# Kernel optimization log

Hardware: AMD Instinct MI355X
Metric: run time of the kernel (lower is better)

Reference implementation:

```python
import jax, jax.numpy as jnp
import numpy as np
from jax import lax

N, C, H, W = 32, 256, 32, 32
E, K, MLP = 8, 2, 4
CAP = 1.25
HID = MLP * C
LN_EPS = 1e-6


def setup_inputs() -> dict:
    key = jax.random.key(0)
    ks = jax.random.split(key, 12)
    s = 0.02
    return {
        "input": jax.random.normal(ks[0], (N, C, H, W), jnp.float32),
        "dw_kernel": jax.random.normal(ks[1], (C, 1, 7, 7), jnp.float32) * s,
        "dw_bias": jnp.zeros((C,), jnp.float32),
        "ln_gamma": jnp.ones((C,), jnp.float32),
        "ln_beta": jnp.zeros((C,), jnp.float32),
        "router_w": jax.random.normal(ks[2], (C, E), jnp.float32) * s,
        "w1": jax.random.normal(ks[3], (E, C, HID), jnp.float32) * s,
        "b1": jnp.zeros((E, HID), jnp.float32),
        "w2": jax.random.normal(ks[4], (E, HID, C), jnp.float32) * s,
        "b2": jnp.zeros((E, C), jnp.float32),
        "layer_scale": jnp.full((C, 1, 1), 1e-6, jnp.float32),
    }


def reference(input, dw_kernel, dw_bias, ln_gamma, ln_beta, router_w,
              w1, b1, w2, b2, layer_scale):
    # depthwise 7x7 conv (groups = C), NCHW
    x = lax.conv_general_dilated(
        input, dw_kernel, window_strides=(1, 1), padding=[(3, 3), (3, 3)],
        dimension_numbers=("NCHW", "OIHW", "NCHW"), feature_group_count=C)
    x = x + dw_bias[None, :, None, None]
    x = jnp.transpose(x, (0, 2, 3, 1))  # NHWC
    # LayerNorm over channels
    mu = jnp.mean(x, axis=-1, keepdims=True)
    var = jnp.mean(jnp.square(x - mu), axis=-1, keepdims=True)
    x = (x - mu) * lax.rsqrt(var + LN_EPS) * ln_gamma + ln_beta

    T = N * H * W
    x_flat = x.reshape(T, C)

    # router (eval mode of NoisyTopKRouter: no noise)
    logits = x_flat @ router_w                      # [T, E]
    top_logits, topi = lax.top_k(logits, K)          # [T, K]
    weights = jax.nn.softmax(top_logits, axis=-1)    # [T, K]
    priority = weights[:, 0]
    order = jnp.argsort(-priority)                   # descending priority

    # build K*T candidates, stably sorted by expert id
    token_idx = jnp.tile(order, K)                           # order.repeat(K)
    expert_id = topi[order].T.reshape(-1)
    gate_w = weights[order].T.reshape(-1)
    perm = jnp.argsort(expert_id)                            # stable
    token_idx, expert_id, gate_w = token_idx[perm], expert_id[perm], gate_w[perm]

    # capacity truncation
    Be = int(K * T * CAP / E + 0.5)
    counts = jnp.bincount(expert_id, length=E)
    starts = jnp.cumsum(counts) - counts
    pos = jnp.arange(K * T) - starts[expert_id]
    keep = pos < Be
    slot = jnp.where(keep, expert_id * Be + pos, E * Be)     # dump slot for drops

    # dispatch to capacity buffers [E, Be, C]
    buf = jnp.zeros((E * Be + 1, C), x_flat.dtype).at[slot].set(x_flat[token_idx])
    buf = buf[:E * Be].reshape(E, Be, C)

    # grouped expert MLP: Linear -> GELU(exact) -> Linear
    h = jax.nn.gelu(jnp.einsum("ebc,ech->ebh", buf, w1) + b1[:, None, :],
                    approximate=False)
    y = jnp.einsum("ebh,ehc->ebc", h, w2) + b2[:, None, :]

    # combine: gather back, gate-scale (zero for dropped), scatter-add
    y_pad = jnp.concatenate([y.reshape(E * Be, C),
                             jnp.zeros((1, C), y.dtype)], axis=0)
    contrib = y_pad[slot] * (gate_w * keep.astype(gate_w.dtype))[:, None]
    out = jnp.zeros((T, C), x_flat.dtype).at[token_idx].add(contrib)

    out = out.reshape(N, H, W, C).transpose(0, 3, 1, 2)      # NCHW
    # stochastic_depth_prob = 0 -> identity
    return input + layer_scale[None] * out
```

## Files before the change

### kernel.cpp

```cpp
#include <hip/hip_runtime.h>
#include <math.h>

#define TOK 32768
#define CH  256
#define HIDN 1024
#define NE  8
#define BE  10240
#define CNT_STRIDE 64

typedef __attribute__((ext_vector_type(8))) short bf16x8;
typedef __attribute__((ext_vector_type(4))) float f32x4;
typedef __attribute__((ext_vector_type(2))) long long2v;

__device__ __forceinline__ unsigned short f2bf(float f) {
    unsigned u = __builtin_bit_cast(unsigned, f);
    unsigned r = 0x7FFFu + ((u >> 16) & 1u);
    return (unsigned short)((u + r) >> 16);
}
__device__ __forceinline__ float bf2f(unsigned short u) {
    return __builtin_bit_cast(float, (unsigned)u << 16);
}
__device__ __forceinline__ unsigned pk8_lo(float a, float b, unsigned old) {
    return (unsigned)__builtin_amdgcn_cvt_pk_fp8_f32(a, b, (int)old, false);
}
__device__ __forceinline__ unsigned pk8_hi(float a, float b, unsigned old) {
    return (unsigned)__builtin_amdgcn_cvt_pk_fp8_f32(a, b, (int)old, true);
}
__device__ __forceinline__ f32x4 mfma8(long a, long b, f32x4 c) {
    return __builtin_amdgcn_mfma_f32_16x16x32_fp8_fp8(a, b, c, 0, 0, 0);
}

typedef __attribute__((address_space(3))) void lds_t;
typedef const __attribute__((address_space(1))) void gm_t;
#define GL16(gp, lp) __builtin_amdgcn_global_load_lds((gm_t*)(gp), (lds_t*)(lp), 16, 0, 0)

__global__ __launch_bounds__(256) void k_conv(const float* __restrict__ in,
                                              const float* __restrict__ kern,
                                              const float* __restrict__ bias,
                                              unsigned char* __restrict__ xc8,
                                              int* __restrict__ cnt) {
    __shared__ float img[1024];
    __shared__ float kwl[49];
    int t = threadIdx.x;
    int bid = blockIdx.x;
    int c = bid & 255;
    if (bid == 0) { cnt[t] = 0; cnt[t + 256] = 0; }

    GL16(in + (size_t)bid * 1024 + t * 4, (char*)img + t * 16);
    if (t < 49) kwl[t] = kern[c * 49 + t];
    __syncthreads();

    int x0 = (t & 7) * 4, y = t >> 3;
    float b0 = bias[c];
    float acc[4] = {b0, b0, b0, b0};
#pragma unroll
    for (int jr = 0; jr < 7; ++jr) {
        int yy = y + jr - 3;
        if ((unsigned)yy < 32u) {
            float row[10];
#pragma unroll
            for (int k = 0; k < 10; ++k) {
                int xx = x0 - 3 + k;
                row[k] = ((unsigned)xx < 32u) ? img[yy * 32 + xx] : 0.f;
            }
#pragma unroll
            for (int kx = 0; kx < 7; ++kx) {
                float kv = kwl[jr * 7 + kx];
#pragma unroll
                for (int o = 0; o < 4; ++o) acc[o] = fmaf(row[o + kx], kv, acc[o]);
            }
        }
    }
    unsigned u = pk8_lo(acc[0], acc[1], 0u);
    u = pk8_hi(acc[2], acc[3], u);
    *(unsigned*)(xc8 + (size_t)bid * 1024 + y * 32 + x0) = u;
}

__global__ __launch_bounds__(512) void k_lnr(const unsigned char* __restrict__ xc8,
                                             const float* __restrict__ gamma,
                                             const float* __restrict__ beta,
                                             const float* __restrict__ rw,
                                             unsigned* __restrict__ xf8,
                                             int* __restrict__ e01,
                                             float2* __restrict__ gates) {
    __shared__ float acc[32][260];
    int t = threadIdx.x;
    int n = blockIdx.x >> 5, y = blockIdx.x & 31;
    int x4 = t & 7, ch = t >> 3;

#pragma unroll
    for (int i = 0; i < 4; ++i) {
        int c = i * 64 + ch;
        unsigned word = *(const unsigned*)(xc8 + ((size_t)(n * 256 + c)) * 1024 + y * 32 + x4 * 4);
        acc[x4 * 4 + 0][c] = __builtin_amdgcn_cvt_f32_fp8((int)word, 0);
        acc[x4 * 4 + 1][c] = __builtin_amdgcn_cvt_f32_fp8((int)word, 1);
        acc[x4 * 4 + 2][c] = __builtin_amdgcn_cvt_f32_fp8((int)word, 2);
        acc[x4 * 4 + 3][c] = __builtin_amdgcn_cvt_f32_fp8((int)word, 3);
    }
    __syncthreads();

    int lane = t & 63, w = t >> 6;
    float4 g4 = ((const float4*)gamma)[lane];
    float4 b4 = ((const float4*)beta)[lane];
    int c0 = lane * 4;
    float4 rwv[8];
#pragma unroll
    for (int j = 0; j < 4; ++j) {
        rwv[j * 2]     = *(const float4*)(rw + (size_t)(c0 + j) * 8);
        rwv[j * 2 + 1] = *(const float4*)(rw + (size_t)(c0 + j) * 8 + 4);
    }

#pragma unroll
    for (int k = 0; k < 4; ++k) {
        int tl = w * 4 + k;
        float4 v = *(const float4*)&acc[tl][lane * 4];
        float s = v.x + v.y + v.z + v.w;
        float q = v.x * v.x + v.y * v.y + v.z * v.z + v.w * v.w;
#pragma unroll
        for (int m = 1; m < 64; m <<= 1) { s += __shfl_xor(s, m); q += __shfl_xor(q, m); }
        float mean = s * (1.0f / 256.0f);
        float var  = q * (1.0f / 256.0f) - mean * mean;
        float rstd = rsqrtf(var + 1e-6f);

        float xn[4];
        xn[0] = (v.x - mean) * rstd * g4.x + b4.x;
        xn[1] = (v.y - mean) * rstd * g4.y + b4.y;
        xn[2] = (v.z - mean) * rstd * g4.z + b4.z;
        xn[3] = (v.w - mean) * rstd * g4.w + b4.w;

        unsigned px = pk8_lo(xn[0], xn[1], 0u);
        px = pk8_hi(xn[2], xn[3], px);
        int tok = n * 1024 + y * 32 + tl;
        xf8[tok * 64 + lane] = px;

        float p[8];
#pragma unroll
        for (int e = 0; e < 8; ++e) p[e] = 0.f;
#pragma unroll
        for (int j = 0; j < 4; ++j) {
            float xv = xn[j];
            const float* r0 = (const float*)&rwv[j * 2];
#pragma unroll
            for (int e = 0; e < 8; ++e) p[e] += xv * r0[e];
        }
#pragma unroll
        for (int m = 1; m < 64; m <<= 1) {
#pragma unroll
            for (int e = 0; e < 8; ++e) p[e] += __shfl_xor(p[e], m);
        }
        if (lane == 0) {
            int e0 = 0; float l0 = p[0];
#pragma unroll
            for (int e = 1; e < 8; ++e) if (p[e] > l0) { l0 = p[e]; e0 = e; }
            int e1 = -1; float l1 = -3.4e38f;
#pragma unroll
            for (int e = 0; e < 8; ++e) if (e != e0 && p[e] > l1) { l1 = p[e]; e1 = e; }
            float tt = expf(l1 - l0);
            float w0 = 1.0f / (1.0f + tt);
            e01[tok] = e0 | (e1 << 8);
            gates[tok] = make_float2(w0, 1.0f - w0);
        }
    }
}

__global__ __launch_bounds__(256) void k_assign(const int* __restrict__ e01,
                                                int* __restrict__ cnt,
                                                int* __restrict__ row_token,
                                                int2* __restrict__ slots) {
    __shared__ int lcnt[8];
    __shared__ int base[8];
    int t = threadIdx.x;
    if (t < 8) lcnt[t] = 0;
    __syncthreads();
    int tok = blockIdx.x * 256 + t;
    int ee = e01[tok];
    int e0 = ee & 255, e1 = (ee >> 8) & 255;
    int lp0 = atomicAdd(&lcnt[e0], 1);
    int lp1 = atomicAdd(&lcnt[e1], 1);
    __syncthreads();
    if (t < 8) base[t] = atomicAdd(cnt + t * CNT_STRIDE, lcnt[t]);
    __syncthreads();
    int pos0 = base[e0] + lp0;
    int pos1 = base[e1] + lp1;
    int slot0 = (pos0 < BE) ? e0 * BE + pos0 : -1;
    int slot1 = (pos1 < BE) ? e1 * BE + pos1 : -1;
    if (slot0 >= 0) row_token[slot0] = tok;
    if (slot1 >= 0) row_token[slot1] = tok;
    slots[tok] = make_int2(slot0, slot1);
}

__global__ __launch_bounds__(256) void k_pack(const float* __restrict__ w1,
                                              const float* __restrict__ w2,
                                              unsigned char* __restrict__ w1p,
                                              unsigned char* __restrict__ w2p) {
    int bid = blockIdx.x;
    int t = threadIdx.x;
    if (bid < 512) {
        int s = bid * 256 + t;
        int l = s & 63, tile = s >> 6;
        int kp = tile & 3, h = (tile >> 2) & 1, hc = (tile >> 3) & 31, e = tile >> 8;
        int l15 = l & 15, l4 = l >> 4;
        int hid = hc * 32 + h * 16 + l15;
        int ch0 = kp * 64 + l4 * 8;
        const float* s0 = w1 + ((size_t)e * 256 + ch0) * 1024 + hid;
        float v[8], u[8];
#pragma unroll
        for (int b = 0; b < 8; ++b) { v[b] = s0[b * 1024]; u[b] = s0[(b + 32) * 1024]; }
        uint4 o;
        o.x = pk8_hi(v[2], v[3], pk8_lo(v[0], v[1], 0u));
        o.y = pk8_hi(v[6], v[7], pk8_lo(v[4], v[5], 0u));
        o.z = pk8_hi(u[2], u[3], pk8_lo(u[0], u[1], 0u));
        o.w = pk8_hi(u[6], u[7], pk8_lo(u[4], u[5], 0u));
        *(uint4*)(w1p + (size_t)tile * 1024 + l * 16) = o;
    } else {
        int s = (bid - 512) * 256 + t;
        int l = s & 63, tile = s >> 6;
        int np = tile & 7, hc = (tile >> 3) & 31, e = tile >> 8;
        int l15 = l & 15, l4 = l >> 4;
        float v[8], u[8];
#pragma unroll
        for (int b = 0; b < 8; ++b) {
            int hidl = ((b >> 2) & 1) * 16 + l4 * 4 + (b & 3);
            const float* s0 = w2 + ((size_t)e * 1024 + hc * 32 + hidl) * 256 + np * 32 + l15;
            v[b] = s0[0];
            u[b] = s0[16];
        }
        uint4 o;
        o.x = pk8_hi(v[2], v[3], pk8_lo(v[0], v[1], 0u));
        o.y = pk8_hi(v[6], v[7], pk8_lo(v[4], v[5], 0u));
        o.z = pk8_hi(u[2], u[3], pk8_lo(u[0], u[1], 0u));
        o.w = pk8_hi(u[6], u[7], pk8_lo(u[4], u[5], 0u));
        *(uint4*)(w2p + (size_t)tile * 1024 + l * 16) = o;
    }
}

__global__ __launch_bounds__(256, 3) void k_mlp(const unsigned char* __restrict__ xf8,
                                                const unsigned char* __restrict__ w1p,
                                                const unsigned char* __restrict__ w2p,
                                                const float* __restrict__ b1,
                                                const float* __restrict__ b2,
                                                const int* __restrict__ cnt,
                                                const int* __restrict__ row_token,
                                                unsigned short* __restrict__ Y) {
    int bid = blockIdx.x;
    int e = bid & 7;
    int row0 = (bid >> 3) * 64;
    int nrows = min(cnt[e * CNT_STRIDE], BE);
    if (row0 >= nrows) return;

    __shared__ char smem[45056];
    char* const W1S0 = smem;
    char* const W1S1 = smem + 8192;
    char* const W2S0 = smem + 16384;
    char* const W2S1 = smem + 24576;
    char* const W2S2 = smem + 32768;
    char* const b1lds = smem + 40960;

    int t = threadIdx.x;
    int w = t >> 6, lane = t & 63;
    int l15 = lane & 15, l4 = lane >> 4;

    const unsigned char* w1e = w1p + (size_t)e * 262144;
    const unsigned char* w2e = w2p + (size_t)e * 262144;

    int ri = row0 + w * 16 + l15;
    int tok0 = (ri < nrows) ? row_token[e * BE + ri] : 0;
    long xr[8];
#pragma unroll
    for (int ks = 0; ks < 8; ++ks)
        xr[ks] = *(const long*)(xf8 + (size_t)tok0 * 256 + ks * 32 + l4 * 8);

    GL16((const char*)(b1 + e * HIDN) + t * 16, b1lds + t * 16);
    GL16(w1e + t * 16, W1S0 + t * 16);
    GL16(w1e + 4096 + t * 16, W1S0 + 4096 + t * 16);
    GL16(w2e + t * 16, W2S0 + t * 16);
    GL16(w2e + 4096 + t * 16, W2S0 + 4096 + t * 16);
    __builtin_amdgcn_sched_barrier(0);
    asm volatile("s_waitcnt vmcnt(2)" ::: "memory");
    __builtin_amdgcn_s_barrier();
    __builtin_amdgcn_sched_barrier(0);

    f32x4 yacc[16];
#pragma unroll
    for (int nc = 0; nc < 16; ++nc) yacc[nc] = f32x4{0.f, 0.f, 0.f, 0.f};

    long hfA = 0, hfB = 0;

    auto STEP = [&](const char* w1c, const char* w2r, char* w1f_, char* w2f_,
                    const unsigned char* g1, const unsigned char* g2,
                    bool doStage, bool doB, long hin, long& hout,
                    int b1off, bool last) {
        if (doStage) {
            GL16(g1 + t * 16, w1f_ + t * 16);
            GL16(g1 + 4096 + t * 16, w1f_ + 4096 + t * 16);
            GL16(g2 + t * 16, w2f_ + t * 16);
            GL16(g2 + 4096 + t * 16, w2f_ + 4096 + t * 16);
        }
        long w1fr[2][8];
#pragma unroll
        for (int h = 0; h < 2; ++h)
#pragma unroll
            for (int kp = 0; kp < 4; ++kp) {
                long2v q = *(const long2v*)(w1c + (h * 4 + kp) * 1024 + lane * 16);
                w1fr[h][kp * 2] = q.x;
                w1fr[h][kp * 2 + 1] = q.y;
            }
        f32x4 ha0 = f32x4{0.f, 0.f, 0.f, 0.f};
        f32x4 ha1 = f32x4{0.f, 0.f, 0.f, 0.f};
#pragma unroll
        for (int ks = 0; ks < 8; ++ks) {
            ha0 = mfma8(w1fr[0][ks], xr[ks], ha0);
            ha1 = mfma8(w1fr[1][ks], xr[ks], ha1);
        }
        if (doB) {
#pragma unroll
            for (int np = 0; np < 8; ++np) {
                long2v q = *(const long2v*)(w2r + np * 1024 + lane * 16);
                yacc[np * 2]     = mfma8(q.x, hin, yacc[np * 2]);
                yacc[np * 2 + 1] = mfma8(q.y, hin, yacc[np * 2 + 1]);
            }
        }
        float4 bv0 = *(const float4*)(b1lds + b1off + l4 * 16);
        float4 bv1 = *(const float4*)(b1lds + b1off + 64 + l4 * 16);
        float g[4];
#pragma unroll
        for (int j = 0; j < 4; ++j) {
            float vv = ha0[j] + ((const float*)&bv0)[j];
            g[j] = vv * __builtin_amdgcn_rcpf(1.0f + __builtin_amdgcn_exp2f(-2.4554672f * vv));
        }
        unsigned p0 = pk8_hi(g[2], g[3], pk8_lo(g[0], g[1], 0u));
#pragma unroll
        for (int j = 0; j < 4; ++j) {
            float vv = ha1[j] + ((const float*)&bv1)[j];
            g[j] = vv * __builtin_amdgcn_rcpf(1.0f + __builtin_amdgcn_exp2f(-2.4554672f * vv));
        }
        unsigned p1 = pk8_hi(g[2], g[3], pk8_lo(g[0], g[1], 0u));
        hout = (long)(((unsigned long)p1 << 32) | (unsigned long)p0);

        __builtin_amdgcn_sched_barrier(0);
        if (last) asm volatile("s_waitcnt vmcnt(0)" ::: "memory");
        else      asm volatile("s_waitcnt vmcnt(2)" ::: "memory");
        __builtin_amdgcn_s_barrier();
        __builtin_amdgcn_sched_barrier(0);
    };

    const char *w1r = W1S0, *w1f = W1S1;
    const char *w2red = W2S2, *w2cur = W2S0, *w2fil = W2S1;
    const unsigned char* g1 = w1e + 8192;
    const unsigned char* g2 = w2e + 8192;
    int b1off = 0;

#define ROTATE() { const char* _a = w1r; w1r = w1f; w1f = _a; \
                   const char* _b = w2red; w2red = w2cur; w2cur = w2fil; w2fil = _b; \
                   g1 += 8192; g2 += 8192; b1off += 128; }

    STEP(w1r, w2red, (char*)w1f, (char*)w2fil, g1, g2, true, false, hfB, hfA, b1off, false);
    ROTATE();
    for (int i = 0; i < 5; ++i) {
        STEP(w1r, w2red, (char*)w1f, (char*)w2fil, g1, g2, true, true, hfA, hfB, b1off, false); ROTATE();
        STEP(w1r, w2red, (char*)w1f, (char*)w2fil, g1, g2, true, true, hfB, hfA, b1off, false); ROTATE();
        STEP(w1r, w2red, (char*)w1f, (char*)w2fil, g1, g2, true, true, hfA, hfB, b1off, false); ROTATE();
        STEP(w1r, w2red, (char*)w1f, (char*)w2fil, g1, g2, true, true, hfB, hfA, b1off, false); ROTATE();
        STEP(w1r, w2red, (char*)w1f, (char*)w2fil, g1, g2, true, true, hfA, hfB, b1off, false); ROTATE();
        STEP(w1r, w2red, (char*)w1f, (char*)w2fil, g1, g2, true, true, hfB, hfA, b1off, false); ROTATE();
    }
    STEP(w1r, w2red, (char*)w1f, (char*)w2fil, g1, g2, false, true, hfA, hfB, b1off, true);
#pragma unroll
    for (int np = 0; np < 8; ++np) {
        long2v q = *(const long2v*)(w2cur + np * 1024 + lane * 16);
        yacc[np * 2]     = mfma8(q.x, hfB, yacc[np * 2]);
        yacc[np * 2 + 1] = mfma8(q.y, hfB, yacc[np * 2 + 1]);
    }
#undef ROTATE

#pragma unroll
    for (int nc = 0; nc < 16; ++nc) {
        float4 bv = *(const float4*)(b2 + e * 256 + nc * 16 + l4 * 4);
#pragma unroll
        for (int jj = 0; jj < 4; ++jj) yacc[nc][jj] += ((const float*)&bv)[jj];
    }
    __syncthreads();
    int lrow = w * 16 + l15;
#pragma unroll
    for (int nc = 0; nc < 16; ++nc) {
#pragma unroll
        for (int jp = 0; jp < 2; ++jp) {
            unsigned pk = (unsigned)f2bf(yacc[nc][jp * 2]) |
                          ((unsigned)f2bf(yacc[nc][jp * 2 + 1]) << 16);
            *(unsigned*)(smem + lrow * 520 + (nc * 16 + l4 * 4 + jp * 2) * 2) = pk;
        }
    }
    __syncthreads();
    {
        char* Yg = (char*)(Y + ((size_t)e * BE + row0) * 256);
#pragma unroll
        for (int i = 0; i < 8; ++i) {
            int flat = i * 4096 + t * 16;
            int row = flat >> 9, off = flat & 511;
            *(int4*)(Yg + row * 512 + off) = *(const int4*)(smem + row * 520 + off);
        }
    }
}

__global__ __launch_bounds__(256) void k_gather(const float* __restrict__ input,
                                                const unsigned short* __restrict__ Y,
                                                const int2* __restrict__ slots,
                                                const float2* __restrict__ gates,
                                                const float* __restrict__ ls,
                                                float* __restrict__ out) {
    __shared__ float acc[32][257];
    int t = threadIdx.x;
    int n = blockIdx.x >> 5, y = blockIdx.x & 31;

    {
        int tl = t & 31, chunk = t >> 5;
        int tok = n * 1024 + y * 32 + tl;
        int2  sl = slots[tok];
        float2 gw = gates[tok];
        int c0 = chunk * 32;
#pragma unroll
        for (int i = 0; i < 4; ++i) {
            int c = c0 + i * 8;
            float v[8];
#pragma unroll
            for (int k = 0; k < 8; ++k) v[k] = 0.f;
            if (sl.x >= 0) {
                bf16x8 yv = *(const bf16x8*)(Y + (size_t)sl.x * 256 + c);
#pragma unroll
                for (int k = 0; k < 8; ++k) v[k] += gw.x * bf2f((unsigned short)yv[k]);
            }
            if (sl.y >= 0) {
                bf16x8 yv = *(const bf16x8*)(Y + (size_t)sl.y * 256 + c);
#pragma unroll
                for (int k = 0; k < 8; ++k) v[k] += gw.y * bf2f((unsigned short)yv[k]);
            }
#pragma unroll
            for (int k = 0; k < 8; ++k) acc[tl][c + k] = v[k];
        }
    }
    __syncthreads();
    {
        int x = t & 31, c8 = t >> 5;
        size_t base = (size_t)n * 256 * 1024 + (size_t)y * 32 + x;
#pragma unroll
        for (int p = 0; p < 32; ++p) {
            int c = p * 8 + c8;
            size_t id = base + (size_t)c * 1024;
            out[id] = input[id] + ls[c] * acc[x][c];
        }
    }
}

extern "C" void kernel_launch(void* const* d_in, const int* in_sizes, int n_in,
                              void* d_out, int out_size, void* d_ws, size_t ws_size,
                              hipStream_t stream) {
    const float* input = (const float*)d_in[0];
    const float* dwk   = (const float*)d_in[1];
    const float* dwb   = (const float*)d_in[2];
    const float* gamma = (const float*)d_in[3];
    const float* beta  = (const float*)d_in[4];
    const float* rw    = (const float*)d_in[5];
    const float* w1    = (const float*)d_in[6];
    const float* b1    = (const float*)d_in[7];
    const float* w2    = (const float*)d_in[8];
    const float* b2    = (const float*)d_in[9];
    const float* ls    = (const float*)d_in[10];

    char* ws = (char*)d_ws;
    unsigned char*  xc8  = (unsigned char*)ws;
    unsigned short* Yb   = (unsigned short*)ws;
    unsigned*       xf8  = (unsigned*)(ws + 83886080);
    unsigned char*  w1p  = (unsigned char*)(ws + 100663296);
    unsigned char*  w2p  = (unsigned char*)(ws + 104857600);
    int*            rtok = (int*)(ws + 109051904);
    int2*           slots = (int2*)(ws + 109379584);
    float2*         gates = (float2*)(ws + 109641728);
    int*            e01  = (int*)(ws + 109903872);
    int*            cnt  = (int*)(ws + 110035968);

    k_conv<<<8192, 256, 0, stream>>>(input, dwk, dwb, xc8, cnt);
    k_lnr<<<1024, 512, 0, stream>>>(xc8, gamma, beta, rw, xf8, e01, gates);
    k_assign<<<128, 256, 0, stream>>>(e01, cnt, rtok, slots);
    k_pack<<<1024, 256, 0, stream>>>(w1, w2, w1p, w2p);
    k_mlp<<<1280, 256, 0, stream>>>((const unsigned char*)xf8, w1p, w2p, b1, b2, cnt, rtok, Yb);
    k_gather<<<1024, 256, 0, stream>>>(input, Yb, slots, gates, ls, (float*)d_out);
}
```

Before: 168.3 us.

## Repartition MLP waves into row-pair x hidden-half tiles with LDS-staged hidden activations

The expert MLP kernel now splits its four waves into two row pairs and two hidden/output halves. Each wave handles 32 rows over half of the hidden chunk, so every W1/W2 fragment read from LDS feeds two MFMAs instead of one. The hidden activations are exchanged through a double-buffered LDS scratch area, which costs extra LDS traffic, a larger shared allocation and an lgkmcnt wait in each step. Separately, the weight-packing kernel is folded into the conv launch as extra blocks, removing one kernel launch, and the W2 packing reads are made contiguous with a new hidden-index mapping.

Result: slower. 184.1 us (+9.4%).

```diff
diff --git a/kernel.cpp b/kernel.cpp
--- a/kernel.cpp
+++ b/kernel.cpp
@@ -37,12 +37,57 @@
 __global__ __launch_bounds__(256) void k_conv(const float* __restrict__ in,
                                               const float* __restrict__ kern,
                                               const float* __restrict__ bias,
+                                              const float* __restrict__ w1,
+                                              const float* __restrict__ w2,
                                               unsigned char* __restrict__ xc8,
+                                              unsigned char* __restrict__ w1p,
+                                              unsigned char* __restrict__ w2p,
                                               int* __restrict__ cnt) {
     __shared__ float img[1024];
     __shared__ float kwl[49];
     int t = threadIdx.x;
     int bid = blockIdx.x;
+
+    if (bid >= 8192) {
+        int pb = bid - 8192;
+        if (pb < 512) {
+            int s = pb * 256 + t;
+            int l = s & 63, tile = s >> 6;
+            int kp = tile & 3, h = (tile >> 2) & 1, hc = (tile >> 3) & 31, e = tile >> 8;
+            int l15 = l & 15, l4 = l >> 4;
+            int hid = hc * 32 + h * 16 + l15;
+            int ch0 = kp * 64 + l4 * 8;
+            const float* s0 = w1 + ((size_t)e * 256 + ch0) * 1024 + hid;
+            float v[8], u[8];
+#pragma unroll
+            for (int b = 0; b < 8; ++b) { v[b] = s0[b * 1024]; u[b] = s0[(b + 32) * 1024]; }
+            uint4 o;
+            o.x = pk8_hi(v[2], v[3], pk8_lo(v[0], v[1], 0u));
+            o.y = pk8_hi(v[6], v[7], pk8_lo(v[4], v[5], 0u));
+            o.z = pk8_hi(u[2], u[3], pk8_lo(u[0], u[1], 0u));
+            o.w = pk8_hi(u[6], u[7], pk8_lo(u[4], u[5], 0u));
+            *(uint4*)(w1p + (size_t)tile * 1024 + l * 16) = o;
+        } else {
+            int s = (pb - 512) * 256 + t;
+            int l = s & 63, tile = s >> 6;
+            int np = tile & 7, hc = (tile >> 3) & 31, e = tile >> 8;
+            int l15 = l & 15, l4 = l >> 4;
+            int hid0 = hc * 32 + l4 * 8;
+            int col0 = np * 32 + l15;
+            const float* s0 = w2 + ((size_t)e * 1024 + hid0) * 256 + col0;
+            float v[8], u[8];
+#pragma unroll
+            for (int b = 0; b < 8; ++b) { v[b] = s0[b * 256]; u[b] = s0[b * 256 + 16]; }
+            uint4 o;
+            o.x = pk8_hi(v[2], v[3], pk8_lo(v[0], v[1], 0u));
+            o.y = pk8_hi(v[6], v[7], pk8_lo(v[4], v[5], 0u));
+            o.z = pk8_hi(u[2], u[3], pk8_lo(u[0], u[1], 0u));
+            o.w = pk8_hi(u[6], u[7], pk8_lo(u[4], u[5], 0u));
+            *(uint4*)(w2p + (size_t)tile * 1024 + l * 16) = o;
+        }
+        return;
+    }
+
     int c = bid & 255;
     if (bid == 0) { cnt[t] = 0; cnt[t + 256] = 0; }
 
@@ -187,51 +232,6 @@
     if (slot0 >= 0) row_token[slot0] = tok;
     if (slot1 >= 0) row_token[slot1] = tok;
     slots[tok] = make_int2(slot0, slot1);
-}
-
-__global__ __launch_bounds__(256) void k_pack(const float* __restrict__ w1,
-                                              const float* __restrict__ w2,
-                                              unsigned char* __restrict__ w1p,
-                                              unsigned char* __restrict__ w2p) {
-    int bid = blockIdx.x;
-    int t = threadIdx.x;
-    if (bid < 512) {
-        int s = bid * 256 + t;
-        int l = s & 63, tile = s >> 6;
-        int kp = tile & 3, h = (tile >> 2) & 1, hc = (tile >> 3) & 31, e = tile >> 8;
-        int l15 = l & 15, l4 = l >> 4;
-        int hid = hc * 32 + h * 16 + l15;
-        int ch0 = kp * 64 + l4 * 8;
-        const float* s0 = w1 + ((size_t)e * 256 + ch0) * 1024 + hid;
-        float v[8], u[8];
-#pragma unroll
-        for (int b = 0; b < 8; ++b) { v[b] = s0[b * 1024]; u[b] = s0[(b + 32) * 1024]; }
-        uint4 o;
-        o.x = pk8_hi(v[2], v[3], pk8_lo(v[0], v[1], 0u));
-        o.y = pk8_hi(v[6], v[7], pk8_lo(v[4], v[5], 0u));
-        o.z = pk8_hi(u[2], u[3], pk8_lo(u[0], u[1], 0u));
-        o.w = pk8_hi(u[6], u[7], pk8_lo(u[4], u[5], 0u));
-        *(uint4*)(w1p + (size_t)tile * 1024 + l * 16) = o;
-    } else {
-        int s = (bid - 512) * 256 + t;
-        int l = s & 63, tile = s >> 6;
-        int np = tile & 7, hc = (tile >> 3) & 31, e = tile >> 8;
-        int l15 = l & 15, l4 = l >> 4;
-        float v[8], u[8];
-#pragma unroll
-        for (int b = 0; b < 8; ++b) {
-            int hidl = ((b >> 2) & 1) * 16 + l4 * 4 + (b & 3);
-            const float* s0 = w2 + ((size_t)e * 1024 + hc * 32 + hidl) * 256 + np * 32 + l15;
-            v[b] = s0[0];
-            u[b] = s0[16];
-        }
-        uint4 o;
-        o.x = pk8_hi(v[2], v[3], pk8_lo(v[0], v[1], 0u));
-        o.y = pk8_hi(v[6], v[7], pk8_lo(v[4], v[5], 0u));
-        o.z = pk8_hi(u[2], u[3], pk8_lo(u[0], u[1], 0u));
-        o.w = pk8_hi(u[6], u[7], pk8_lo(u[4], u[5], 0u));
-        *(uint4*)(w2p + (size_t)tile * 1024 + l * 16) = o;
-    }
 }
 
 __global__ __launch_bounds__(256, 3) void k_mlp(const unsigned char* __restrict__ xf8,
@@ -248,27 +248,32 @@
     int nrows = min(cnt[e * CNT_STRIDE], BE);
     if (row0 >= nrows) return;
 
-    __shared__ char smem[45056];
+    __shared__ char smem[49664];
     char* const W1S0 = smem;
     char* const W1S1 = smem + 8192;
     char* const W2S0 = smem + 16384;
     char* const W2S1 = smem + 24576;
     char* const W2S2 = smem + 32768;
     char* const b1lds = smem + 40960;
+    char* const Hbase = smem + 45056;
 
     int t = threadIdx.x;
     int w = t >> 6, lane = t & 63;
     int l15 = lane & 15, l4 = lane >> 4;
+    int p = w >> 1, s = w & 1;
 
     const unsigned char* w1e = w1p + (size_t)e * 262144;
     const unsigned char* w2e = w2p + (size_t)e * 262144;
 
-    int ri = row0 + w * 16 + l15;
-    int tok0 = (ri < nrows) ? row_token[e * BE + ri] : 0;
-    long xr[8];
-#pragma unroll
-    for (int ks = 0; ks < 8; ++ks)
-        xr[ks] = *(const long*)(xf8 + (size_t)tok0 * 256 + ks * 32 + l4 * 8);
+    int ri = row0 + p * 32 + l15;
+    int tokA = (ri < nrows) ? row_token[e * BE + ri] : 0;
+    int tokB = (ri + 16 < nrows) ? row_token[e * BE + ri + 16] : 0;
+    long xr[2][8];
+#pragma unroll
+    for (int ks = 0; ks < 8; ++ks) {
+        xr[0][ks] = *(const long*)(xf8 + (size_t)tokA * 256 + ks * 32 + l4 * 8);
+        xr[1][ks] = *(const long*)(xf8 + (size_t)tokB * 256 + ks * 32 + l4 * 8);
+    }
 
     GL16((const char*)(b1 + e * HIDN) + t * 16, b1lds + t * 16);
     GL16(w1e + t * 16, W1S0 + t * 16);
@@ -284,11 +289,9 @@
 #pragma unroll
     for (int nc = 0; nc < 16; ++nc) yacc[nc] = f32x4{0.f, 0.f, 0.f, 0.f};
 
-    long hfA = 0, hfB = 0;
-
     auto STEP = [&](const char* w1c, const char* w2r, char* w1f_, char* w2f_,
                     const unsigned char* g1, const unsigned char* g2,
-                    bool doStage, bool doB, long hin, long& hout,
+                    bool doStage, bool doB, const char* hR, char* hW,
                     int b1off, bool last) {
         if (doStage) {
             GL16(g1 + t * 16, w1f_ + t * 16);
@@ -296,53 +299,58 @@
             GL16(g2 + t * 16, w2f_ + t * 16);
             GL16(g2 + 4096 + t * 16, w2f_ + 4096 + t * 16);
         }
-        long w1fr[2][8];
-#pragma unroll
-        for (int h = 0; h < 2; ++h)
-#pragma unroll
-            for (int kp = 0; kp < 4; ++kp) {
-                long2v q = *(const long2v*)(w1c + (h * 4 + kp) * 1024 + lane * 16);
-                w1fr[h][kp * 2] = q.x;
-                w1fr[h][kp * 2 + 1] = q.y;
-            }
+        long w1fr[8];
+#pragma unroll
+        for (int kp = 0; kp < 4; ++kp) {
+            long2v q = *(const long2v*)(w1c + (s * 4 + kp) * 1024 + lane * 16);
+            w1fr[kp * 2] = q.x;
+            w1fr[kp * 2 + 1] = q.y;
+        }
         f32x4 ha0 = f32x4{0.f, 0.f, 0.f, 0.f};
         f32x4 ha1 = f32x4{0.f, 0.f, 0.f, 0.f};
 #pragma unroll
         for (int ks = 0; ks < 8; ++ks) {
-            ha0 = mfma8(w1fr[0][ks], xr[ks], ha0);
-            ha1 = mfma8(w1fr[1][ks], xr[ks], ha1);
+            ha0 = mfma8(w1fr[ks], xr[0][ks], ha0);
+            ha1 = mfma8(w1fr[ks], xr[1][ks], ha1);
         }
         if (doB) {
-#pragma unroll
-            for (int np = 0; np < 8; ++np) {
-                long2v q = *(const long2v*)(w2r + np * 1024 + lane * 16);
-                yacc[np * 2]     = mfma8(q.x, hin, yacc[np * 2]);
-                yacc[np * 2 + 1] = mfma8(q.y, hin, yacc[np * 2 + 1]);
+            long hb0 = *(const long*)(hR + p * 1152 + l15 * 36 + l4 * 8);
+            long hb1 = *(const long*)(hR + p * 1152 + (16 + l15) * 36 + l4 * 8);
+#pragma unroll
+            for (int jp = 0; jp < 4; ++jp) {
+                long2v q = *(const long2v*)(w2r + (s * 4 + jp) * 1024 + lane * 16);
+                yacc[jp * 4 + 0] = mfma8(q.x, hb0, yacc[jp * 4 + 0]);
+                yacc[jp * 4 + 1] = mfma8(q.x, hb1, yacc[jp * 4 + 1]);
+                yacc[jp * 4 + 2] = mfma8(q.y, hb0, yacc[jp * 4 + 2]);
+                yacc[jp * 4 + 3] = mfma8(q.y, hb1, yacc[jp * 4 + 3]);
             }
         }
-        float4 bv0 = *(const float4*)(b1lds + b1off + l4 * 16);
-        float4 bv1 = *(const float4*)(b1lds + b1off + 64 + l4 * 16);
+        float4 bv = *(const float4*)(b1lds + b1off + s * 64 + l4 * 16);
         float g[4];
 #pragma unroll
         for (int j = 0; j < 4; ++j) {
-            float vv = ha0[j] + ((const float*)&bv0)[j];
+            float vv = ha0[j] + ((const float*)&bv)[j];
             g[j] = vv * __builtin_amdgcn_rcpf(1.0f + __builtin_amdgcn_exp2f(-2.4554672f * vv));
         }
-        unsigned p0 = pk8_hi(g[2], g[3], pk8_lo(g[0], g[1], 0u));
+        unsigned pk0 = pk8_hi(g[2], g[3], pk8_lo(g[0], g[1], 0u));
 #pragma unroll
         for (int j = 0; j < 4; ++j) {
-            float vv = ha1[j] + ((const float*)&bv1)[j];
+            float vv = ha1[j] + ((const float*)&bv)[j];
             g[j] = vv * __builtin_amdgcn_rcpf(1.0f + __builtin_amdgcn_exp2f(-2.4554672f * vv));
         }
-        unsigned p1 = pk8_hi(g[2], g[3], pk8_lo(g[0], g[1], 0u));
-        hout = (long)(((unsigned long)p1 << 32) | (unsigned long)p0);
+        unsigned pk1 = pk8_hi(g[2], g[3], pk8_lo(g[0], g[1], 0u));
+        *(unsigned*)(hW + p * 1152 + l15 * 36 + s * 16 + l4 * 4) = pk0;
+        *(unsigned*)(hW + p * 1152 + (16 + l15) * 36 + s * 16 + l4 * 4) = pk1;
 
         __builtin_amdgcn_sched_barrier(0);
-        if (last) asm volatile("s_waitcnt vmcnt(0)" ::: "memory");
-        else      asm volatile("s_waitcnt vmcnt(2)" ::: "memory");
+        if (last) asm volatile("s_waitcnt vmcnt(0) lgkmcnt(0)" ::: "memory");
+        else      asm volatile("s_waitcnt vmcnt(2) lgkmcnt(0)" ::: "memory");
         __builtin_amdgcn_s_barrier();
         __builtin_amdgcn_sched_barrier(0);
     };
+
+    char* const H0 = Hbase;
+    char* const H1 = Hbase + 2304;
 
     const char *w1r = W1S0, *w1f = W1S1;
     const char *w2red = W2S2, *w2cur = W2S0, *w2fil = W2S1;
@@ -354,40 +362,52 @@
                    const char* _b = w2red; w2red = w2cur; w2cur = w2fil; w2fil = _b; \
                    g1 += 8192; g2 += 8192; b1off += 128; }
 
-    STEP(w1r, w2red, (char*)w1f, (char*)w2fil, g1, g2, true, false, hfB, hfA, b1off, false);
+    STEP(w1r, w2red, (char*)w1f, (char*)w2fil, g1, g2, true, false, H1, H0, b1off, false);
     ROTATE();
     for (int i = 0; i < 5; ++i) {
-        STEP(w1r, w2red, (char*)w1f, (char*)w2fil, g1, g2, true, true, hfA, hfB, b1off, false); ROTATE();
-        STEP(w1r, w2red, (char*)w1f, (char*)w2fil, g1, g2, true, true, hfB, hfA, b1off, false); ROTATE();
-        STEP(w1r, w2red, (char*)w1f, (char*)w2fil, g1, g2, true, true, hfA, hfB, b1off, false); ROTATE();
-        STEP(w1r, w2red, (char*)w1f, (char*)w2fil, g1, g2, true, true, hfB, hfA, b1off, false); ROTATE();
-        STEP(w1r, w2red, (char*)w1f, (char*)w2fil, g1, g2, true, true, hfA, hfB, b1off, false); ROTATE();
-        STEP(w1r, w2red, (char*)w1f, (char*)w2fil, g1, g2, true, true, hfB, hfA, b1off, false); ROTATE();
-    }
-    STEP(w1r, w2red, (char*)w1f, (char*)w2fil, g1, g2, false, true, hfA, hfB, b1off, true);
-#pragma unroll
-    for (int np = 0; np < 8; ++np) {
-        long2v q = *(const long2v*)(w2cur + np * 1024 + lane * 16);
-        yacc[np * 2]     = mfma8(q.x, hfB, yacc[np * 2]);
-        yacc[np * 2 + 1] = mfma8(q.y, hfB, yacc[np * 2 + 1]);
+        STEP(w1r, w2red, (char*)w1f, (char*)w2fil, g1, g2, true, true, H0, H1, b1off, false); ROTATE();
+        STEP(w1r, w2red, (char*)w1f, (char*)w2fil, g1, g2, true, true, H1, H0, b1off, false); ROTATE();
+        STEP(w1r, w2red, (char*)w1f, (char*)w2fil, g1, g2, true, true, H0, H1, b1off, false); ROTATE();
+        STEP(w1r, w2red, (char*)w1f, (char*)w2fil, g1, g2, true, true, H1, H0, b1off, false); ROTATE();
+        STEP(w1r, w2red, (char*)w1f, (char*)w2fil, g1, g2, true, true, H0, H1, b1off, false); ROTATE();
+        STEP(w1r, w2red, (char*)w1f, (char*)w2fil, g1, g2, true, true, H1, H0, b1off, false); ROTATE();
+    }
+    STEP(w1r, w2red, (char*)w1f, (char*)w2fil, g1, g2, false, true, H0, H1, b1off, true);
+    {
+        long hb0 = *(const long*)(H1 + p * 1152 + l15 * 36 + l4 * 8);
+        long hb1 = *(const long*)(H1 + p * 1152 + (16 + l15) * 36 + l4 * 8);
+        asm volatile("s_waitcnt lgkmcnt(0)" ::: "memory");
+        __builtin_amdgcn_sched_barrier(0);
+#pragma unroll
+        for (int jp = 0; jp < 4; ++jp) {
+            long2v q = *(const long2v*)(w2cur + (s * 4 + jp) * 1024 + lane * 16);
+            yacc[jp * 4 + 0] = mfma8(q.x, hb0, yacc[jp * 4 + 0]);
+            yacc[jp * 4 + 1] = mfma8(q.x, hb1, yacc[jp * 4 + 1]);
+            yacc[jp * 4 + 2] = mfma8(q.y, hb0, yacc[jp * 4 + 2]);
+            yacc[jp * 4 + 3] = mfma8(q.y, hb1, yacc[jp * 4 + 3]);
+        }
     }
 #undef ROTATE
 
-#pragma unroll
-    for (int nc = 0; nc < 16; ++nc) {
-        float4 bv = *(const float4*)(b2 + e * 256 + nc * 16 + l4 * 4);
-#pragma unroll
-        for (int jj = 0; jj < 4; ++jj) yacc[nc][jj] += ((const float*)&bv)[jj];
-    }
-    __syncthreads();
-    int lrow = w * 16 + l15;
-#pragma unroll
-    for (int nc = 0; nc < 16; ++nc) {
-#pragma unroll
-        for (int jp = 0; jp < 2; ++jp) {
-            unsigned pk = (unsigned)f2bf(yacc[nc][jp * 2]) |
-                          ((unsigned)f2bf(yacc[nc][jp * 2 + 1]) << 16);
-            *(unsigned*)(smem + lrow * 520 + (nc * 16 + l4 * 4 + jp * 2) * 2) = pk;
+    __syncthreads();
+#pragma unroll
+    for (int jp = 0; jp < 4; ++jp) {
+#pragma unroll
+        for (int half = 0; half < 2; ++half) {
+            int outb = s * 128 + jp * 32 + half * 16 + l4 * 4;
+            float4 bv = *(const float4*)(b2 + e * 256 + outb);
+#pragma unroll
+            for (int tf = 0; tf < 2; ++tf) {
+                f32x4 av = yacc[jp * 4 + half * 2 + tf];
+                int lrow = p * 32 + tf * 16 + l15;
+#pragma unroll
+                for (int jq = 0; jq < 2; ++jq) {
+                    float a0 = av[jq * 2] + ((const float*)&bv)[jq * 2];
+                    float a1 = av[jq * 2 + 1] + ((const float*)&bv)[jq * 2 + 1];
+                    unsigned pkv = (unsigned)f2bf(a0) | ((unsigned)f2bf(a1) << 16);
+                    *(unsigned*)(smem + lrow * 520 + (outb + jq * 2) * 2) = pkv;
+                }
+            }
         }
     }
     __syncthreads();
@@ -478,10 +498,9 @@
     int*            e01  = (int*)(ws + 109903872);
     int*            cnt  = (int*)(ws + 110035968);
 
-    k_conv<<<8192, 256, 0, stream>>>(input, dwk, dwb, xc8, cnt);
+    k_conv<<<9216, 256, 0, stream>>>(input, dwk, dwb, w1, w2, xc8, w1p, w2p, cnt);
     k_lnr<<<1024, 512, 0, stream>>>(xc8, gamma, beta, rw, xf8, e01, gates);
     k_assign<<<128, 256, 0, stream>>>(e01, cnt, rtok, slots);
-    k_pack<<<1024, 256, 0, stream>>>(w1, w2, w1p, w2p);
     k_mlp<<<1280, 256, 0, stream>>>((const unsigned char*)xf8, w1p, w2p, b1, b2, cnt, rtok, Yb);
     k_gather<<<1024, 256, 0, stream>>>(input, Yb, slots, gates, ls, (float*)d_out);
 }
```
